# Performance work log

Measured on AMD Instinct MI355X. Metric: run time of the kernel, lower is better.

The kernel has to match this reference:

```python
import jax, jax.numpy as jnp
import numpy as np

KERNEL = 3
STRIDE = 1
PADDING = 1
DILATION = 1
GRID_SIZE = 3
SPLINE_ORDER = 2
IN_CH = 3
OUT_CH = 32
IN_FEAT = IN_CH * KERNEL * KERNEL  # 27
N_BASIS = GRID_SIZE + SPLINE_ORDER  # 5


def _make_grid():
    # efficient-kan grid: uniform knots over [-1, 1] extended by spline_order on each side
    h = 2.0 / GRID_SIZE
    g = np.arange(-SPLINE_ORDER, GRID_SIZE + SPLINE_ORDER + 1, dtype=np.float32) * h - 1.0
    return jnp.asarray(np.broadcast_to(g, (IN_FEAT, g.shape[0])))  # (27, 8)


def b_splines(x, grid):
    # x: (N, F); grid: (F, G). Cox-de Boor recursion.
    x = x[:, :, None]                      # (N, F, 1)
    g = grid[None, :, :]                   # (1, F, G)
    bases = ((x >= g[..., :-1]) & (x < g[..., 1:])).astype(x.dtype)
    for k in range(1, SPLINE_ORDER + 1):
        bases = ((x - g[..., : -(k + 1)]) / (g[..., k:-1] - g[..., : -(k + 1)]) * bases[..., :-1]
                 + (g[..., k + 1:] - x) / (g[..., k + 1:] - g[..., 1:-k]) * bases[..., 1:])
    return bases  # (N, F, N_BASIS)


def setup_inputs() -> dict:
    key = jax.random.key(0)
    k1, k2, k3, k4 = jax.random.split(key, 4)
    x = jax.random.normal(k1, (16, IN_CH, 256, 256), dtype=jnp.float32)
    # Kaiming-ish init scales (values irrelevant for correctness testing)
    base_weight = jax.random.normal(k2, (OUT_CH, IN_FEAT), dtype=jnp.float32) * (1.0 / np.sqrt(IN_FEAT))
    spline_weight = jax.random.normal(k3, (OUT_CH, IN_FEAT, N_BASIS), dtype=jnp.float32) * 0.1
    spline_scaler = jax.random.normal(k4, (OUT_CH, IN_FEAT), dtype=jnp.float32) * (1.0 / np.sqrt(IN_FEAT))
    grid = _make_grid()
    return {"x": x, "base_weight": base_weight, "spline_weight": spline_weight,
            "spline_scaler": spline_scaler, "grid": grid}


def reference(x, base_weight, spline_weight, spline_scaler, grid):
    B, C, H, W = x.shape
    out_h = (H + 2 * PADDING - DILATION * (KERNEL - 1) - 1) // STRIDE + 1
    out_w = (W + 2 * PADDING - DILATION * (KERNEL - 1) - 1) // STRIDE + 1
    # im2col: (B, C*k*k, out_h, out_w), feature ordering (C, kh, kw) matches torch Unfold
    patches = jax.lax.conv_general_dilated_patches(
        x, filter_shape=(KERNEL, KERNEL), window_strides=(STRIDE, STRIDE),
        padding=((PADDING, PADDING), (PADDING, PADDING)), rhs_dilation=(DILATION, DILATION))
    pf = patches.reshape(B, IN_FEAT, out_h * out_w).transpose(0, 2, 1).reshape(-1, IN_FEAT)  # (N, 27)
    # KANLinear: silu base branch + scaled spline branch
    base = jnp.einsum('nf,of->no', jax.nn.silu(pf), base_weight)
    bases = b_splines(pf, grid)                                   # (N, 27, 5)
    scaled_sw = spline_weight * spline_scaler[:, :, None]         # (O, 27, 5)
    spline = jnp.einsum('nfk,ofk->no', bases, scaled_sw)
    out = base + spline                                           # (N, O)
    return out.reshape(B, out_h * out_w, OUT_CH).transpose(0, 2, 1).reshape(B, OUT_CH, out_h, out_w)
```

## Files before the change

kernel.cpp:

```cpp
#include <hip/hip_runtime.h>

#define IN_CH 3
#define OUT_CH 32
#define IN_FEAT 27
#define NB 5
#define NG 8
#define HH 256
#define WW 256
#define NPIX (16 * HH * WW)

#define RECE 24
#define RECP 28
#define TW 66
#define TROWS 6
#define NREC (TROWS * TW)
#define WB_HALVES (9 * 2 * 64 * 8)
#define GTAB_FLOATS 21
#define WS_NEEDED ((size_t)WB_HALVES * 2 + GTAB_FLOATS * 4)

typedef __attribute__((ext_vector_type(8))) _Float16 half8;
typedef __attribute__((ext_vector_type(4))) float f32x4;
typedef __attribute__((ext_vector_type(4))) unsigned int u32x4;

__device__ inline void kan_phi6(float xx, const float* g, const float* r1, const float* r2,
                                float* o6) {
    const float sig = 1.0f / (1.0f + __expf(-xx));
    o6[0] = xx * sig;
    float b0[7];
#pragma unroll
    for (int j = 0; j < 7; ++j) b0[j] = (xx >= g[j] && xx < g[j + 1]) ? 1.0f : 0.0f;
    float b1[6];
#pragma unroll
    for (int j = 0; j < 6; ++j)
        b1[j] = (xx - g[j]) * r1[j] * b0[j] + (g[j + 2] - xx) * r1[j + 1] * b0[j + 1];
#pragma unroll
    for (int j = 0; j < NB; ++j)
        o6[1 + j] = (xx - g[j]) * r2[j] * b1[j] + (g[j + 3] - xx) * r2[j + 1] * b1[j + 1];
}

__device__ inline void load_grid(const float* __restrict__ grid, float* g, float* r1, float* r2) {
#pragma unroll
    for (int j = 0; j < NG; ++j) g[j] = grid[j];
#pragma unroll
    for (int j = 0; j < NG - 1; ++j) r1[j] = 1.0f / (g[j + 1] - g[j]);
#pragma unroll
    for (int j = 0; j < NG - 2; ++j) r2[j] = 1.0f / (g[j + 2] - g[j]);
}

__global__ void kan_prepW(const float* __restrict__ bw, const float* __restrict__ sw,
                          const float* __restrict__ ss, const float* __restrict__ grid,
                          _Float16* __restrict__ wb) {
    int t = blockIdx.x * 256 + threadIdx.x;
    if (t >= 9 * 2 * 64) return;

    if (t == 0) {
        float g[NG], r1[NG - 1], r2[NG - 2];
        load_grid(grid, g, r1, r2);
        float* gt = (float*)(wb + WB_HALVES);
#pragma unroll
        for (int j = 0; j < NG; ++j) gt[j] = g[j];
#pragma unroll
        for (int j = 0; j < NG - 1; ++j) gt[NG + j] = r1[j];
#pragma unroll
        for (int j = 0; j < NG - 2; ++j) gt[NG + NG - 1 + j] = r2[j];
    }

    const int lane = t & 63;
    const int nt = (t >> 6) & 1;
    const int tap = t >> 7;
    const int o = nt * 16 + (lane & 15);
    const int kbase = (lane >> 4) * 8;
    half8 v8 = {0, 0, 0, 0, 0, 0, 0, 0};
#pragma unroll
    for (int e = 0; e < 8; ++e) {
        int kk = kbase + e;
        float v = 0.0f;
        if (kk < 18) {
            int c = kk / 6, j = kk % 6;
            int f = c * 9 + tap;
            int of = o * IN_FEAT + f;
            v = (j == 0) ? bw[of] : sw[of * NB + (j - 1)] * ss[of];
        }
        v8[e] = (_Float16)v;
    }
    *(half8*)(wb + (size_t)t * 8) = v8;
}

__global__ __launch_bounds__(256) void kan_fused(const float* __restrict__ x,
                                                 const _Float16* __restrict__ wb,
                                                 float* __restrict__ out) {
    __shared__ _Float16 lPhi[NREC * RECP];

    const int tid = threadIdx.x;
    const int bid = blockIdx.x;
    const int strip = bid & 3;
    const int rowg = (bid >> 2) & 63;
    const int b = bid >> 8;
    const int h0 = rowg * 4;
    const int w0 = strip * 64;

    const int lane = tid & 63;
    const int wid = tid >> 6;
    const int r = lane & 15;
    const int gq = lane >> 4;

    half8 bf[18];
#pragma unroll
    for (int i = 0; i < 18; ++i)
        bf[i] = *(const half8*)(wb + ((size_t)(i * 64 + lane)) * 8);

    const float* gt = (const float*)(wb + WB_HALVES);
    float g[NG], r1[NG - 1], r2[NG - 2];
#pragma unroll
    for (int j = 0; j < NG; ++j) g[j] = gt[j];
#pragma unroll
    for (int j = 0; j < NG - 1; ++j) r1[j] = gt[NG + j];
#pragma unroll
    for (int j = 0; j < NG - 2; ++j) r2[j] = gt[NG + NG - 1 + j];

    for (int rr = tid; rr < NREC; rr += 256) {
        const int dyR = rr / TW;
        const int wxR = rr - dyR * TW - 1;
        const int hy = h0 + dyR - 1;
        const int wx = w0 + wxR;
        const bool vld = ((unsigned)hy < HH) & ((unsigned)wx < WW);

        _Float16 rec[RECE];
#pragma unroll
        for (int c = 0; c < IN_CH; ++c) {
            const float xx = vld ? x[((b * IN_CH + c) << 16) + (hy << 8) + wx] : 0.0f;
            float o6[6];
            kan_phi6(xx, g, r1, r2, o6);
#pragma unroll
            for (int j = 0; j < 6; ++j) rec[c * 6 + j] = (_Float16)o6[j];
        }
#pragma unroll
        for (int j = 18; j < RECE; ++j) rec[j] = (_Float16)0.0f;

        half8* dst = (half8*)(lPhi + rr * RECP);
        dst[0] = *(half8*)(rec + 0);
        dst[1] = *(half8*)(rec + 8);
        dst[2] = *(half8*)(rec + 16);
    }
    __syncthreads();

    const int hrow = h0 + wid;
#pragma unroll
    for (int m = 0; m < 4; ++m) {
        half8 af[9];
#pragma unroll
        for (int dy = 0; dy < 3; ++dy) {
#pragma unroll
            for (int dx = 0; dx < 3; ++dx) {
                const int rec = (wid + dy) * TW + m * 16 + r + dx;
                half8 v = {0, 0, 0, 0, 0, 0, 0, 0};
                if (gq < 3) v = *(const half8*)(lPhi + rec * RECP + gq * 8);
                af[dy * 3 + dx] = v;
            }
        }

        f32x4 acc0 = {0.f, 0.f, 0.f, 0.f};
        f32x4 acc1 = {0.f, 0.f, 0.f, 0.f};
#pragma unroll
        for (int tap = 0; tap < 9; ++tap) {
            acc0 = __builtin_amdgcn_mfma_f32_16x16x32_f16(af[tap], bf[tap * 2 + 0], acc0, 0, 0, 0);
            acc1 = __builtin_amdgcn_mfma_f32_16x16x32_f16(af[tap], bf[tap * 2 + 1], acc1, 0, 0, 0);
        }

        const int wcol = w0 + m * 16 + gq * 4;
        float* op0 = out + ((size_t)(b * OUT_CH + r) << 16) + (hrow << 8) + wcol;
        float* op1 = out + ((size_t)(b * OUT_CH + 16 + r) << 16) + (hrow << 8) + wcol;
        *(f32x4*)op0 = acc0;
        *(f32x4*)op1 = acc1;
    }
}

__global__ void kan_combine_weights(const float* __restrict__ bw,
                                    const float* __restrict__ sw,
                                    const float* __restrict__ ss,
                                    float* __restrict__ wc) {
    int idx = blockIdx.x * blockDim.x + threadIdx.x;
    if (idx >= IN_FEAT * 6 * OUT_CH) return;
    int o = idx & 31;
    int j = (idx >> 5) % 6;
    int f = idx / (6 * 32);
    float v;
    if (j == 0) v = bw[o * IN_FEAT + f];
    else        v = sw[(o * IN_FEAT + f) * NB + (j - 1)] * ss[o * IN_FEAT + f];
    wc[idx] = v;
}

__global__ __launch_bounds__(256) void kan_main(const float* __restrict__ x,
                                                const float* __restrict__ grid,
                                                const float* __restrict__ wc,
                                                float* __restrict__ out) {
    const int p = blockIdx.x * blockDim.x + threadIdx.x;
    const int w = p & (WW - 1);
    const int h = (p >> 8) & (HH - 1);
    const int b = p >> 16;
    float g[NG], r1[NG - 1], r2[NG - 2];
    load_grid(grid, g, r1, r2);
    float acc[OUT_CH];
#pragma unroll
    for (int o = 0; o < OUT_CH; ++o) acc[o] = 0.0f;
    const float* xb = x + b * (IN_CH * HH * WW);
    for (int c = 0; c < IN_CH; ++c) {
        const float* xc = xb + c * (HH * WW);
#pragma unroll
        for (int dy = 0; dy < 3; ++dy) {
            const int hy = h + dy - 1;
            const bool vy = (hy >= 0) && (hy < HH);
#pragma unroll
            for (int dx = 0; dx < 3; ++dx) {
                const int wx = w + dx - 1;
                const bool vld = vy && (wx >= 0) && (wx < WW);
                const float xx = vld ? xc[hy * WW + wx] : 0.0f;
                float o6[6];
                kan_phi6(xx, g, r1, r2, o6);
                const float* wf = wc + (c * 9 + dy * 3 + dx) * (6 * OUT_CH);
#pragma unroll
                for (int jj = 0; jj < 6; ++jj) {
                    const float* wj = wf + jj * OUT_CH;
#pragma unroll
                    for (int o = 0; o < OUT_CH; ++o) acc[o] += o6[jj] * wj[o];
                }
            }
        }
    }
    float* ob = out + (size_t)b * (OUT_CH * HH * WW) + h * WW + w;
#pragma unroll
    for (int o = 0; o < OUT_CH; ++o) ob[o * (HH * WW)] = acc[o];
}

extern "C" void kernel_launch(void* const* d_in, const int* in_sizes, int n_in,
                              void* d_out, int out_size, void* d_ws, size_t ws_size,
                              hipStream_t stream) {
    const float* x    = (const float*)d_in[0];
    const float* bw   = (const float*)d_in[1];
    const float* sw   = (const float*)d_in[2];
    const float* ss   = (const float*)d_in[3];
    const float* grid = (const float*)d_in[4];
    float* out = (float*)d_out;

    if (ws_size >= WS_NEEDED) {
        _Float16* wb = (_Float16*)d_ws;
        kan_prepW<<<(9 * 2 * 64 + 255) / 256, 256, 0, stream>>>(bw, sw, ss, grid, wb);
        kan_fused<<<NPIX / 256, 256, 0, stream>>>(x, wb, out);
    } else {
        float* wc = (float*)d_ws;
        kan_combine_weights<<<(IN_FEAT * 6 * OUT_CH + 255) / 256, 256, 0, stream>>>(bw, sw, ss, wc);
        kan_main<<<NPIX / 256, 256, 0, stream>>>(x, grid, wc, out);
    }
}
```

Before: 47.53 us.

## Double rows per block, reuse tap rows across outputs, closed-form uniform B-spline

Each block now covers 8 output rows instead of 4, so the halo overhead in the phi tile drops from 6 to 10 rows for twice the output. Each wave computes two output rows, and the loaded row fragments are reused across vertically adjacent taps, which cuts LDS reads per output. The Cox-de Boor recursion is replaced by a closed-form uniform quadratic B-spline (floor index plus three weights), using only the grid origin and inverse spacing. This assumes uniform knots and halves the grid count, which could reduce occupancy at small batch.

```diff
diff --git a/kernel.cpp b/kernel.cpp
--- a/kernel.cpp
+++ b/kernel.cpp
@@ -12,11 +12,10 @@
 #define RECE 24
 #define RECP 28
 #define TW 66
-#define TROWS 6
+#define TROWS 10
 #define NREC (TROWS * TW)
 #define WB_HALVES (9 * 2 * 64 * 8)
-#define GTAB_FLOATS 21
-#define WS_NEEDED ((size_t)WB_HALVES * 2 + GTAB_FLOATS * 4)
+#define WS_NEEDED ((size_t)WB_HALVES * 2 + 16)
 
 typedef __attribute__((ext_vector_type(8))) _Float16 half8;
 typedef __attribute__((ext_vector_type(4))) float f32x4;
@@ -54,15 +53,9 @@
     if (t >= 9 * 2 * 64) return;
 
     if (t == 0) {
-        float g[NG], r1[NG - 1], r2[NG - 2];
-        load_grid(grid, g, r1, r2);
         float* gt = (float*)(wb + WB_HALVES);
-#pragma unroll
-        for (int j = 0; j < NG; ++j) gt[j] = g[j];
-#pragma unroll
-        for (int j = 0; j < NG - 1; ++j) gt[NG + j] = r1[j];
-#pragma unroll
-        for (int j = 0; j < NG - 2; ++j) gt[NG + NG - 1 + j] = r2[j];
+        gt[0] = grid[0];
+        gt[1] = 7.0f / (grid[7] - grid[0]);
     }
 
     const int lane = t & 63;
@@ -94,9 +87,9 @@
     const int tid = threadIdx.x;
     const int bid = blockIdx.x;
     const int strip = bid & 3;
-    const int rowg = (bid >> 2) & 63;
-    const int b = bid >> 8;
-    const int h0 = rowg * 4;
+    const int rowg = (bid >> 2) & 31;
+    const int b = bid >> 7;
+    const int h0 = rowg * 8;
     const int w0 = strip * 64;
 
     const int lane = tid & 63;
@@ -110,17 +103,12 @@
         bf[i] = *(const half8*)(wb + ((size_t)(i * 64 + lane)) * 8);
 
     const float* gt = (const float*)(wb + WB_HALVES);
-    float g[NG], r1[NG - 1], r2[NG - 2];
-#pragma unroll
-    for (int j = 0; j < NG; ++j) g[j] = gt[j];
-#pragma unroll
-    for (int j = 0; j < NG - 1; ++j) r1[j] = gt[NG + j];
-#pragma unroll
-    for (int j = 0; j < NG - 2; ++j) r2[j] = gt[NG + NG - 1 + j];
-
-    for (int rr = tid; rr < NREC; rr += 256) {
-        const int dyR = rr / TW;
-        const int wxR = rr - dyR * TW - 1;
+    const float g0 = gt[0];
+    const float invh = gt[1];
+
+    for (int ri = tid; ri < NREC; ri += 256) {
+        const int dyR = ri / TW;
+        const int wxR = ri - dyR * TW - 1;
         const int hy = h0 + dyR - 1;
         const int wx = w0 + wxR;
         const bool vld = ((unsigned)hy < HH) & ((unsigned)wx < WW);
@@ -129,49 +117,77 @@
 #pragma unroll
         for (int c = 0; c < IN_CH; ++c) {
             const float xx = vld ? x[((b * IN_CH + c) << 16) + (hy << 8) + wx] : 0.0f;
-            float o6[6];
-            kan_phi6(xx, g, r1, r2, o6);
-#pragma unroll
-            for (int j = 0; j < 6; ++j) rec[c * 6 + j] = (_Float16)o6[j];
+            const float sig = 1.0f / (1.0f + __expf(-xx));
+            rec[c * 6] = (_Float16)(xx * sig);
+            const float u = (xx - g0) * invh;
+            const float fi = floorf(u);
+            const int i0 = (int)fi;
+            const float t = u - fi;
+            const float om = 1.0f - t;
+            float wA = 0.5f * om * om;
+            float wC = 0.5f * t * t;
+            float wB = 1.0f - wA - wC;
+            const bool valid = (fi >= 0.0f) & (i0 <= 6);
+            wA = valid ? wA : 0.0f;
+            wB = valid ? wB : 0.0f;
+            wC = valid ? wC : 0.0f;
+#pragma unroll
+            for (int j = 0; j < NB; ++j) {
+                float v = (j == i0 - 2) ? wA : ((j == i0 - 1) ? wB : ((j == i0) ? wC : 0.0f));
+                rec[c * 6 + 1 + j] = (_Float16)v;
+            }
         }
 #pragma unroll
         for (int j = 18; j < RECE; ++j) rec[j] = (_Float16)0.0f;
 
-        half8* dst = (half8*)(lPhi + rr * RECP);
+        half8* dst = (half8*)(lPhi + ri * RECP);
         dst[0] = *(half8*)(rec + 0);
         dst[1] = *(half8*)(rec + 8);
         dst[2] = *(half8*)(rec + 16);
     }
     __syncthreads();
 
-    const int hrow = h0 + wid;
+    const int row0 = wid * 2;
+    const int hr0 = h0 + row0;
 #pragma unroll
     for (int m = 0; m < 4; ++m) {
-        half8 af[9];
+        half8 haf[4][3];
+#pragma unroll
+        for (int hr = 0; hr < 4; ++hr) {
+#pragma unroll
+            for (int dx = 0; dx < 3; ++dx) {
+                const int ridx = (row0 + hr) * TW + m * 16 + r + dx;
+                half8 v = {0, 0, 0, 0, 0, 0, 0, 0};
+                if (gq < 3) v = *(const half8*)(lPhi + ridx * RECP + gq * 8);
+                haf[hr][dx] = v;
+            }
+        }
+
+        f32x4 a00 = {0.f, 0.f, 0.f, 0.f};
+        f32x4 a01 = {0.f, 0.f, 0.f, 0.f};
+        f32x4 a10 = {0.f, 0.f, 0.f, 0.f};
+        f32x4 a11 = {0.f, 0.f, 0.f, 0.f};
 #pragma unroll
         for (int dy = 0; dy < 3; ++dy) {
 #pragma unroll
             for (int dx = 0; dx < 3; ++dx) {
-                const int rec = (wid + dy) * TW + m * 16 + r + dx;
-                half8 v = {0, 0, 0, 0, 0, 0, 0, 0};
-                if (gq < 3) v = *(const half8*)(lPhi + rec * RECP + gq * 8);
-                af[dy * 3 + dx] = v;
-            }
-        }
-
-        f32x4 acc0 = {0.f, 0.f, 0.f, 0.f};
-        f32x4 acc1 = {0.f, 0.f, 0.f, 0.f};
-#pragma unroll
-        for (int tap = 0; tap < 9; ++tap) {
-            acc0 = __builtin_amdgcn_mfma_f32_16x16x32_f16(af[tap], bf[tap * 2 + 0], acc0, 0, 0, 0);
-            acc1 = __builtin_amdgcn_mfma_f32_16x16x32_f16(af[tap], bf[tap * 2 + 1], acc1, 0, 0, 0);
+                const int tap = dy * 3 + dx;
+                a00 = __builtin_amdgcn_mfma_f32_16x16x32_f16(haf[dy][dx],     bf[tap * 2 + 0], a00, 0, 0, 0);
+                a01 = __builtin_amdgcn_mfma_f32_16x16x32_f16(haf[dy][dx],     bf[tap * 2 + 1], a01, 0, 0, 0);
+                a10 = __builtin_amdgcn_mfma_f32_16x16x32_f16(haf[dy + 1][dx], bf[tap * 2 + 0], a10, 0, 0, 0);
+                a11 = __builtin_amdgcn_mfma_f32_16x16x32_f16(haf[dy + 1][dx], bf[tap * 2 + 1], a11, 0, 0, 0);
+            }
         }
 
         const int wcol = w0 + m * 16 + gq * 4;
-        float* op0 = out + ((size_t)(b * OUT_CH + r) << 16) + (hrow << 8) + wcol;
-        float* op1 = out + ((size_t)(b * OUT_CH + 16 + r) << 16) + (hrow << 8) + wcol;
-        *(f32x4*)op0 = acc0;
-        *(f32x4*)op1 = acc1;
+        float* p00 = out + ((size_t)(b * OUT_CH + r) << 16)      + (hr0 << 8)       + wcol;
+        float* p01 = out + ((size_t)(b * OUT_CH + 16 + r) << 16) + (hr0 << 8)       + wcol;
+        float* p10 = out + ((size_t)(b * OUT_CH + r) << 16)      + ((hr0 + 1) << 8) + wcol;
+        float* p11 = out + ((size_t)(b * OUT_CH + 16 + r) << 16) + ((hr0 + 1) << 8) + wcol;
+        *(f32x4*)p00 = a00;
+        *(f32x4*)p01 = a01;
+        *(f32x4*)p10 = a10;
+        *(f32x4*)p11 = a11;
     }
 }
 
@@ -245,7 +261,7 @@
     if (ws_size >= WS_NEEDED) {
         _Float16* wb = (_Float16*)d_ws;
         kan_prepW<<<(9 * 2 * 64 + 255) / 256, 256, 0, stream>>>(bw, sw, ss, grid, wb);
-        kan_fused<<<NPIX / 256, 256, 0, stream>>>(x, wb, out);
+        kan_fused<<<NPIX / 512, 256, 0, stream>>>(x, wb, out);
     } else {
         float* wc = (float*)d_ws;
         kan_combine_weights<<<(IN_FEAT * 6 * OUT_CH + 255) / 256, 256, 0, stream>>>(bw, sw, ss, wc);
```

After: 49.69 us. +4.5%, slower.
